# Optimization experiments

Hardware: AMD Instinct MI355X
Metric: run time of the kernel (lower is better)

## Reference

```python
import jax, jax.numpy as jnp
import numpy as np

N_ENT = 50000
N_EDGE = 600000
FEAT = 128
HID = 256
OUT = 128
TOTAL_RELS = 2 * 50 + 1  # 2*num_relations + 1
BN_EPS = 1e-5


def setup_inputs() -> dict:
    key = jax.random.key(0)
    ks = jax.random.split(key, 14)

    def xavier(k, shape):
        fan_in, fan_out = shape[0], shape[1]
        bound = float(np.sqrt(6.0 / (fan_in + fan_out)))
        return jax.random.uniform(k, shape, jnp.float32, -bound, bound)

    return {
        "edge_index": jax.random.randint(ks[0], (2, N_EDGE), 0, N_ENT, jnp.int32),
        "edge_type": jax.random.randint(ks[1], (N_EDGE,), 0, TOTAL_RELS, jnp.int32),
        "initial_features": xavier(ks[2], (N_ENT, FEAT)),
        "relation_embeddings": xavier(ks[3], (TOTAL_RELS, FEAT)),
        "W_msg": xavier(ks[4], (FEAT, HID)),
        "b_msg": jnp.zeros((HID,), jnp.float32),
        "W_self": xavier(ks[5], (FEAT, HID)),
        "W1": xavier(ks[6], (HID, HID)),
        "b1": jnp.zeros((HID,), jnp.float32),
        "gamma": jnp.ones((HID,), jnp.float32),
        "beta": jnp.zeros((HID,), jnp.float32),
        "W2": xavier(ks[7], (HID, OUT)),
        "b2": jnp.zeros((OUT,), jnp.float32),
    }


def _forward(edge_index, edge_type, initial_features, relation_embeddings,
             W_msg, b_msg, W_self, W1, b1, gamma, beta, W2, b2):
    x = initial_features                                  # [N, F]
    src, dst = edge_index[0], edge_index[1]

    # Relation-aware message: gather source feature + relation embedding per edge.
    msg = x[src] + relation_embeddings[edge_type]         # [E, F]

    # Degree-normalized scatter aggregation (mean over incoming edges).
    agg = jax.ops.segment_sum(msg, dst, num_segments=N_ENT)           # [N, F]
    deg = jax.ops.segment_sum(jnp.ones((msg.shape[0],), msg.dtype), dst,
                              num_segments=N_ENT)                     # [N]
    agg = agg / jnp.maximum(deg, 1.0)[:, None]

    # RelationGCN layer: transformed aggregate + self-loop path.
    h = agg @ W_msg + x @ W_self + b_msg                  # [N, H]

    # semantic_projector: Linear -> BatchNorm1d (batch stats) -> ReLU -> Linear.
    y = h @ W1 + b1                                       # [N, H]
    mean = jnp.mean(y, axis=0)
    var = jnp.var(y, axis=0)
    y = (y - mean) * jax.lax.rsqrt(var + BN_EPS) * gamma + beta
    y = jax.nn.relu(y)
    # Dropout omitted (deterministic reference).
    out = y @ W2 + b2                                     # [N, O]
    return out


def reference(edge_index, edge_type, initial_features, relation_embeddings,
              W_msg, b_msg, W_self, W1, b1, gamma, beta, W2, b2):
    return _forward(edge_index, edge_type, initial_features, relation_embeddings,
                    W_msg, b_msg, W_self, W1, b1, gamma, beta, W2, b2)
```

## Files before the change

kernel.cpp:

```cpp
#include <hip/hip_runtime.h>
#include <hip/hip_bf16.h>

#define N_ENT   50000
#define N_EDGE  600000
#define FEAT    128
#define HID     256
#define OUT_D   128
#define MROWS   50048
#define BN_EPS  1e-5f
#define NT32    (MROWS / 32)
#define RED_BLKS 196
#define NBUCK   196
#define EPB     4096
#define NBLK_E  147

#define OFF_SCALE   202048
#define OFF_SHIFT   203072
#define OFF_RELB    204096
#define OFF_WT1     229952
#define OFF_W1T     361024
#define OFF_W2T     492096
#define OFF_A       557632
#define OFF_Y       26182208
#define OFF_PB      52000000
#define OFF_PB2     55210000
#define OFF_ROWPTR  56000000
#define OFF_PACKED  56400064
#define OFF_EBUF    58900000
#define OFF_CHIST   61300000
#define OFF_OFFA    61420000
#define OFF_CBASE   61540000

typedef __attribute__((ext_vector_type(8))) short bf16x8;
typedef __attribute__((ext_vector_type(4))) float f32x4;

#define GLL(gp, lp) __builtin_amdgcn_global_load_lds( \
    (const __attribute__((address_space(1))) void*)(gp), \
    (__attribute__((address_space(3))) void*)(lp), 16, 0, 0)

#define MFMA(a, b, c) __builtin_amdgcn_mfma_f32_16x16x32_bf16((a), (b), (c), 0, 0, 0)

__device__ __forceinline__ ushort f2bf(float f) {
    uint u = __float_as_uint(f);
    return (ushort)((u + 0x7FFFu + ((u >> 16) & 1u)) >> 16);
}
__device__ __forceinline__ float bflo(uint u) { return __uint_as_float(u << 16); }
__device__ __forceinline__ float bfhi(uint u) { return __uint_as_float(u & 0xFFFF0000u); }

__global__ __launch_bounds__(256) void k_prep(
    const float* __restrict__ x,
    const float* __restrict__ Wm, const float* __restrict__ Wsf,
    const float* __restrict__ W1, const float* __restrict__ W2,
    const float* __restrict__ rel,
    ushort* __restrict__ A,
    ushort* __restrict__ Wt1, ushort* __restrict__ W1t,
    ushort* __restrict__ W2t, ushort* __restrict__ relb)
{
    int b = blockIdx.x;
    if (b < 3125) {
        int idx = b * 256 + threadIdx.x;
        int m = idx >> 4;
        int c = (idx & 15) * 8;
        float4 f0 = *(const float4*)(x + m * FEAT + c);
        float4 f1 = *(const float4*)(x + m * FEAT + c + 4);
        uint4 o;
        o.x = (uint)f2bf(f0.x) | ((uint)f2bf(f0.y) << 16);
        o.y = (uint)f2bf(f0.z) | ((uint)f2bf(f0.w) << 16);
        o.z = (uint)f2bf(f1.x) | ((uint)f2bf(f1.y) << 16);
        o.w = (uint)f2bf(f1.z) | ((uint)f2bf(f1.w) << 16);
        *(uint4*)(A + m * 256 + FEAT + c) = o;
    } else {
        int idx = (b - 3125) * 256 + threadIdx.x;
        if (idx < 65536) {
            int n = idx >> 8, k = idx & 255;
            float v = (k < FEAT) ? Wm[k * HID + n] : Wsf[(k - FEAT) * HID + n];
            int w = n >> 6, nb = (n >> 4) & 3, lr = n & 15;
            int kk = k >> 5, lk = (k >> 3) & 3, j = k & 7;
            int l = lk * 16 + lr;
            Wt1[(((w * 8 + kk) * 4 + nb) * 64 + l) * 8 + j] = f2bf(v);
        } else if (idx < 131072) {
            int o = idx - 65536;
            int n = o >> 8, k = o & 255;
            float v = W1[k * HID + n];
            int w = n >> 6, nb = (n >> 4) & 3, lr = n & 15;
            int kk = k >> 5, lk = (k >> 3) & 3, j = k & 7;
            int l = lk * 16 + lr;
            W1t[(((w * 8 + kk) * 4 + nb) * 64 + l) * 8 + j] = f2bf(v);
        } else if (idx < 163840) {
            int o = idx - 131072;
            int n = o >> 8, k = o & 255;
            float v = W2[k * OUT_D + n];
            int w = n >> 5, nb = (n >> 4) & 1, lr = n & 15;
            int kk = k >> 5, lk = (k >> 3) & 3, j = k & 7;
            int l = lk * 16 + lr;
            W2t[(((w * 8 + kk) * 2 + nb) * 64 + l) * 8 + j] = f2bf(v);
        } else if (idx < 163840 + 101 * 128) {
            int o = idx - 163840;
            relb[o] = f2bf(rel[o]);
        }
    }
}

__global__ __launch_bounds__(256) void k_chist(
    const int* __restrict__ ei, int* __restrict__ chist)
{
    __shared__ int h[NBUCK];
    int t = threadIdx.x;
    if (t < NBUCK) h[t] = 0;
    __syncthreads();
    #pragma unroll
    for (int r = 0; r < 16; ++r) {
        int e = (blockIdx.x * 16 + r) * 256 + t;
        if (e < N_EDGE) atomicAdd(&h[ei[N_EDGE + e] >> 8], 1);
    }
    __syncthreads();
    if (t < NBUCK) chist[blockIdx.x * NBUCK + t] = h[t];
}

__global__ __launch_bounds__(256) void k_cscan(
    const int* __restrict__ chist, int* __restrict__ offa, int* __restrict__ cbase)
{
    __shared__ int s[256];
    int k = threadIdx.x;
    int acc = 0;
    if (k < NBUCK) {
        #pragma unroll 4
        for (int b = 0; b < NBLK_E; ++b) {
            offa[b * NBUCK + k] = acc;
            acc += chist[b * NBUCK + k];
        }
    }
    s[k] = (k < NBUCK) ? acc : 0;
    int v = s[k];
    __syncthreads();
    for (int off = 1; off < 256; off <<= 1) {
        int u = (k >= off) ? s[k - off] : 0;
        __syncthreads();
        s[k] += u;
        __syncthreads();
    }
    if (k < NBUCK) cbase[k] = s[k] - v;
    if (k == NBUCK - 1) cbase[NBUCK] = s[k];
}

__global__ __launch_bounds__(256) void k_cscat(
    const int* __restrict__ ei, const int* __restrict__ et,
    const int* __restrict__ offa, const int* __restrict__ cbase,
    int* __restrict__ ebuf)
{
    __shared__ int base[NBUCK];
    int t = threadIdx.x;
    if (t < NBUCK) base[t] = offa[blockIdx.x * NBUCK + t] + cbase[t];
    __syncthreads();
    #pragma unroll
    for (int r = 0; r < 16; ++r) {
        int e = (blockIdx.x * 16 + r) * 256 + t;
        if (e < N_EDGE) {
            int dst = ei[N_EDGE + e];
            int k = dst >> 8;
            int pos = atomicAdd(&base[k], 1);
            ebuf[pos] = ei[e] | (et[e] << 16) | ((dst & 255) << 23);
        }
    }
}

__global__ __launch_bounds__(256) void k_fine(
    const int* __restrict__ ebuf, const int* __restrict__ cbase,
    int* __restrict__ rowptr, int* __restrict__ packed)
{
    __shared__ int cnt[256], sc[256];
    int t = threadIdx.x, b = blockIdx.x;
    int s0 = cbase[b], s1 = cbase[b + 1];
    cnt[t] = 0;
    __syncthreads();
    for (int e = s0 + t; e < s1; e += 256)
        atomicAdd(&cnt[(ebuf[e] >> 23) & 255], 1);
    __syncthreads();
    int v = cnt[t];
    sc[t] = v;
    __syncthreads();
    for (int off = 1; off < 256; off <<= 1) {
        int u = (t >= off) ? sc[t - off] : 0;
        __syncthreads();
        sc[t] += u;
        __syncthreads();
    }
    int ex = sc[t] - v;
    int node = b * 256 + t;
    if (node < N_ENT) rowptr[node] = s0 + ex;
    if (b == NBUCK - 1 && t == 0) rowptr[N_ENT] = s1;
    __syncthreads();
    cnt[t] = s0 + ex;
    __syncthreads();
    for (int e = s0 + t; e < s1; e += 256) {
        int v32 = ebuf[e];
        int pos = atomicAdd(&cnt[(v32 >> 23) & 255], 1);
        packed[pos] = v32 & 0x7FFFFF;
    }
}

__global__ __launch_bounds__(256) void k_agg(
    const int* __restrict__ rowptr, const int* __restrict__ packed,
    ushort* __restrict__ A, const ushort* __restrict__ relb)
{
    int node = blockIdx.x * 4 + (threadIdx.x >> 6);
    int lane = threadIdx.x & 63;
    int e0 = rowptr[node], e1 = rowptr[node + 1];
    float ax = 0.f, ay = 0.f;
    int e = e0;
    for (; e + 8 <= e1; e += 8) {
        int p0 = packed[e],     p1 = packed[e + 1], p2 = packed[e + 2], p3 = packed[e + 3];
        int p4 = packed[e + 4], p5 = packed[e + 5], p6 = packed[e + 6], p7 = packed[e + 7];
        uint xv0 = *(const uint*)(A + (p0 & 0xFFFF) * 256 + FEAT + lane * 2);
        uint rv0 = *(const uint*)(relb + (p0 >> 16) * FEAT + lane * 2);
        uint xv1 = *(const uint*)(A + (p1 & 0xFFFF) * 256 + FEAT + lane * 2);
        uint rv1 = *(const uint*)(relb + (p1 >> 16) * FEAT + lane * 2);
        uint xv2 = *(const uint*)(A + (p2 & 0xFFFF) * 256 + FEAT + lane * 2);
        uint rv2 = *(const uint*)(relb + (p2 >> 16) * FEAT + lane * 2);
        uint xv3 = *(const uint*)(A + (p3 & 0xFFFF) * 256 + FEAT + lane * 2);
        uint rv3 = *(const uint*)(relb + (p3 >> 16) * FEAT + lane * 2);
        uint xv4 = *(const uint*)(A + (p4 & 0xFFFF) * 256 + FEAT + lane * 2);
        uint rv4 = *(const uint*)(relb + (p4 >> 16) * FEAT + lane * 2);
        uint xv5 = *(const uint*)(A + (p5 & 0xFFFF) * 256 + FEAT + lane * 2);
        uint rv5 = *(const uint*)(relb + (p5 >> 16) * FEAT + lane * 2);
        uint xv6 = *(const uint*)(A + (p6 & 0xFFFF) * 256 + FEAT + lane * 2);
        uint rv6 = *(const uint*)(relb + (p6 >> 16) * FEAT + lane * 2);
        uint xv7 = *(const uint*)(A + (p7 & 0xFFFF) * 256 + FEAT + lane * 2);
        uint rv7 = *(const uint*)(relb + (p7 >> 16) * FEAT + lane * 2);
        ax += bflo(xv0) + bflo(rv0) + bflo(xv1) + bflo(rv1)
            + bflo(xv2) + bflo(rv2) + bflo(xv3) + bflo(rv3)
            + bflo(xv4) + bflo(rv4) + bflo(xv5) + bflo(rv5)
            + bflo(xv6) + bflo(rv6) + bflo(xv7) + bflo(rv7);
        ay += bfhi(xv0) + bfhi(rv0) + bfhi(xv1) + bfhi(rv1)
            + bfhi(xv2) + bfhi(rv2) + bfhi(xv3) + bfhi(rv3)
            + bfhi(xv4) + bfhi(rv4) + bfhi(xv5) + bfhi(rv5)
            + bfhi(xv6) + bfhi(rv6) + bfhi(xv7) + bfhi(rv7);
    }
    for (; e + 4 <= e1; e += 4) {
        int p0 = packed[e], p1 = packed[e + 1], p2 = packed[e + 2], p3 = packed[e + 3];
        uint xv0 = *(const uint*)(A + (p0 & 0xFFFF) * 256 + FEAT + lane * 2);
        uint rv0 = *(const uint*)(relb + (p0 >> 16) * FEAT + lane * 2);
        uint xv1 = *(const uint*)(A + (p1 & 0xFFFF) * 256 + FEAT + lane * 2);
        uint rv1 = *(const uint*)(relb + (p1 >> 16) * FEAT + lane * 2);
        uint xv2 = *(const uint*)(A + (p2 & 0xFFFF) * 256 + FEAT + lane * 2);
        uint rv2 = *(const uint*)(relb + (p2 >> 16) * FEAT + lane * 2);
        uint xv3 = *(const uint*)(A + (p3 & 0xFFFF) * 256 + FEAT + lane * 2);
        uint rv3 = *(const uint*)(relb + (p3 >> 16) * FEAT + lane * 2);
        ax += bflo(xv0) + bflo(rv0) + bflo(xv1) + bflo(rv1)
            + bflo(xv2) + bflo(rv2) + bflo(xv3) + bflo(rv3);
        ay += bfhi(xv0) + bfhi(rv0) + bfhi(xv1) + bfhi(rv1)
            + bfhi(xv2) + bfhi(rv2) + bfhi(xv3) + bfhi(rv3);
    }
    for (; e + 2 <= e1; e += 2) {
        int p0 = packed[e], p1 = packed[e + 1];
        uint xv0 = *(const uint*)(A + (p0 & 0xFFFF) * 256 + FEAT + lane * 2);
        uint rv0 = *(const uint*)(relb + (p0 >> 16) * FEAT + lane * 2);
        uint xv1 = *(const uint*)(A + (p1 & 0xFFFF) * 256 + FEAT + lane * 2);
        uint rv1 = *(const uint*)(relb + (p1 >> 16) * FEAT + lane * 2);
        ax += bflo(xv0) + bflo(rv0) + bflo(xv1) + bflo(rv1);
        ay += bfhi(xv0) + bfhi(rv0) + bfhi(xv1) + bfhi(rv1);
    }
    if (e < e1) {
        int p = packed[e];
        uint xv = *(const uint*)(A + (p & 0xFFFF) * 256 + FEAT + lane * 2);
        uint rv = *(const uint*)(relb + (p >> 16) * FEAT + lane * 2);
        ax += bflo(xv) + bflo(rv);
        ay += bfhi(xv) + bfhi(rv);
    }
    float invd = 1.0f / fmaxf((float)(e1 - e0), 1.0f);
    uint o = (uint)f2bf(ax * invd) | ((uint)f2bf(ay * invd) << 16);
    *(uint*)(A + node * 256 + lane * 2) = o;
}

__global__ __launch_bounds__(256) void k_hy(
    const ushort* __restrict__ A, const ushort* __restrict__ Wt1,
    const ushort* __restrict__ W1t,
    const float* __restrict__ bm, const float* __restrict__ b1,
    ushort* __restrict__ y, float* __restrict__ pb)
{
    __shared__ ushort a_s[32 * 256];
    int tid = threadIdx.x;
    int w = tid >> 6, l = tid & 63;
    int lr = l & 15, lk = l >> 4;
    int m0 = blockIdx.x * 32;

    {
        const ushort* srcb = A + (size_t)m0 * 256;
        #pragma unroll
        for (int j = 0; j < 4; ++j) {
            int slot = (w * 4 + j) * 64 + l;
            int lrow = slot >> 5, lgr = slot & 31;
            GLL(srcb + lrow * 256 + ((lgr ^ (lrow & 7)) << 3), &a_s[(w * 4 + j) * 512]);
        }
    }
    __syncthreads();

    f32x4 acc[2][4] = {};
    const ushort* Bp = Wt1 + w * 16384 + l * 8;
    #pragma unroll
    for (int kk = 0; kk < 8; ++kk) {
        bf16x8 a[2], b[4];
        #pragma unroll
        for (int mb = 0; mb < 2; ++mb) {
            int row = mb * 16 + lr;
            a[mb] = *(const bf16x8*)&a_s[row * 256 + (((kk * 4 + lk) ^ (lr & 7)) << 3)];
        }
        #pragma unroll
        for (int nb = 0; nb < 4; ++nb) b[nb] = *(const bf16x8*)(Bp + kk * 2048 + nb * 512);
        #pragma unroll
        for (int mb = 0; mb < 2; ++mb)
            #pragma unroll
            for (int nb = 0; nb < 4; ++nb)
                acc[mb][nb] = MFMA(a[mb], b[nb], acc[mb][nb]);
    }
    __syncthreads();

    #pragma unroll
    for (int nb = 0; nb < 4; ++nb) {
        int col = w * 64 + nb * 16 + lr;
        float bias = bm[col];
        #pragma unroll
        for (int mb = 0; mb < 2; ++mb)
            #pragma unroll
            for (int r = 0; r < 4; ++r) {
                int row = mb * 16 + lk * 4 + r;
                a_s[row * 256 + (col ^ ((row & 7) << 3))] = f2bf(acc[mb][nb][r] + bias);
            }
    }
    __syncthreads();

    f32x4 acc2[2][4] = {};
    const ushort* B2p = W1t + w * 16384 + l * 8;
    #pragma unroll
    for (int kk = 0; kk < 8; ++kk) {
        bf16x8 a[2], b[4];
        #pragma unroll
        for (int mb = 0; mb < 2; ++mb) {
            int row = mb * 16 + lr;
            a[mb] = *(const bf16x8*)&a_s[row * 256 + ((kk * 32 + lk * 8) ^ ((row & 7) << 3))];
        }
        #pragma unroll
        for (int nb = 0; nb < 4; ++nb) b[nb] = *(const bf16x8*)(B2p + kk * 2048 + nb * 512);
        #pragma unroll
        for (int mb = 0; mb < 2; ++mb)
            #pragma unroll
            for (int nb = 0; nb < 4; ++nb)
                acc2[mb][nb] = MFMA(a[mb], b[nb], acc2[mb][nb]);
    }
    __syncthreads();

    #pragma unroll
    for (int nb = 0; nb < 4; ++nb) {
        int col = w * 64 + nb * 16 + lr;
        float b1v = b1[col];
        float cs = 0.f, cq = 0.f;
        #pragma unroll
        for (int mb = 0; mb < 2; ++mb)
            #pragma unroll
            for (int r = 0; r < 4; ++r) {
                int row = mb * 16 + lk * 4 + r;
                float v = acc2[mb][nb][r] + b1v;
                if (m0 + row < N_ENT) { cs += v; cq += v * v; }
                a_s[row * 256 + (col ^ ((row & 7) << 3))] = f2bf(v);
            }
        cs += __shfl_xor(cs, 16); cs += __shfl_xor(cs, 32);
        cq += __shfl_xor(cq, 16); cq += __shfl_xor(cq, 32);
        if (lk == 0) {
            *(float2*)(pb + (size_t)blockIdx.x * 512 + col * 2) = make_float2(cs, cq);
        }
    }
    __syncthreads();
    ushort* yp = y + (size_t)m0 * 256;
    #pragma unroll
    for (int i = 0; i < 4; ++i) {
        int off = i * 2048 + tid * 8;
        *(uint4*)(yp + off) = *(const uint4*)&a_s[off];
    }
}

__global__ __launch_bounds__(256) void k_red1(
    const float* __restrict__ pb, float* __restrict__ pb2)
{
    int b = blockIdx.x, tid = threadIdx.x;
    int t0 = b * 8;
    float sx = 0.f, sy = 0.f;
    #pragma unroll
    for (int i = 0; i < 8; ++i) {
        int t = t0 + i;
        if (t < NT32) {
            float2 v = *(const float2*)(pb + (size_t)t * 512 + tid * 2);
            sx += v.x; sy += v.y;
        }
    }
    *(float2*)(pb2 + (size_t)b * 512 + tid * 2) = make_float2(sx, sy);
}

__global__ __launch_bounds__(256) void k_red2(
    const float* __restrict__ pb2,
    const float* __restrict__ gamma, const float* __restrict__ beta,
    float* __restrict__ scale, float* __restrict__ shift)
{
    int c = threadIdx.x;
    float s = 0.f, q = 0.f;
    int b = 0;
    #pragma unroll
    for (; b + 8 <= RED_BLKS; b += 8) {
        float2 v0 = *(const float2*)(pb2 + (size_t)(b + 0) * 512 + c * 2);
        float2 v1 = *(const float2*)(pb2 + (size_t)(b + 1) * 512 + c * 2);
        float2 v2 = *(const float2*)(pb2 + (size_t)(b + 2) * 512 + c * 2);
        float2 v3 = *(const float2*)(pb2 + (size_t)(b + 3) * 512 + c * 2);
        float2 v4 = *(const float2*)(pb2 + (size_t)(b + 4) * 512 + c * 2);
        float2 v5 = *(const float2*)(pb2 + (size_t)(b + 5) * 512 + c * 2);
        float2 v6 = *(const float2*)(pb2 + (size_t)(b + 6) * 512 + c * 2);
        float2 v7 = *(const float2*)(pb2 + (size_t)(b + 7) * 512 + c * 2);
        s += v0.x + v1.x + v2.x + v3.x + v4.x + v5.x + v6.x + v7.x;
        q += v0.y + v1.y + v2.y + v3.y + v4.y + v5.y + v6.y + v7.y;
    }
    for (; b < RED_BLKS; ++b) {
        float2 v = *(const float2*)(pb2 + (size_t)b * 512 + c * 2);
        s += v.x; q += v.y;
    }
    const float invn = 1.0f / (float)N_ENT;
    float mean = s * invn;
    float var  = q * invn - mean * mean;
    float rstd = rsqrtf(var + BN_EPS);
    float sc   = gamma[c] * rstd;
    scale[c] = sc;
    shift[c] = beta[c] - mean * sc;
}

__global__ __launch_bounds__(256) void k_zout(
    const ushort* __restrict__ y, const float* __restrict__ scale,
    const float* __restrict__ shift, const ushort* __restrict__ W2t,
    const float* __restrict__ b2, float* __restrict__ out)
{
    __shared__ ushort z_s[32 * 256];
    int tid = threadIdx.x;
    int w = tid >> 6, l = tid & 63;
    int lr = l & 15, lk = l >> 4;
    int m0 = blockIdx.x * 32;

    {
        const ushort* srcb = y + (size_t)m0 * 256;
        #pragma unroll
        for (int j = 0; j < 4; ++j)
            GLL(srcb + ((w * 4 + j) * 64 + l) * 8, &z_s[(w * 4 + j) * 512]);
    }
    __syncthreads();

    f32x4 acc[2][2] = {};
    const ushort* Bp = W2t + w * 8192 + l * 8;
    #pragma unroll
    for (int kk = 0; kk < 8; ++kk) {
        int kb = kk * 32 + lk * 8;
        float scv[8], shv[8];
        *(float4*)&scv[0] = *(const float4*)(scale + kb);
        *(float4*)&scv[4] = *(const float4*)(scale + kb + 4);
        *(float4*)&shv[0] = *(const float4*)(shift + kb);
        *(float4*)&shv[4] = *(const float4*)(shift + kb + 4);
        bf16x8 b[2];
        #pragma unroll
        for (int nb = 0; nb < 2; ++nb) b[nb] = *(const bf16x8*)(Bp + kk * 1024 + nb * 512);
        bf16x8 a[2];
        #pragma unroll
        for (int mb = 0; mb < 2; ++mb) {
            int row = mb * 16 + lr;
            uint4 uv = *(const uint4*)&z_s[row * 256 + (kb ^ ((row & 7) << 3))];
            uint wd[4] = {uv.x, uv.y, uv.z, uv.w};
            #pragma unroll
            for (int j = 0; j < 8; ++j) {
                uint bits = (j & 1) ? (wd[j >> 1] & 0xFFFF0000u) : (wd[j >> 1] << 16);
                float f = __uint_as_float(bits);
                float z = fmaxf(f * scv[j] + shv[j], 0.f);
                a[mb][j] = (short)f2bf(z);
            }
        }
        #pragma unroll
        for (int mb = 0; mb < 2; ++mb)
            #pragma unroll
            for (int nb = 0; nb < 2; ++nb)
                acc[mb][nb] = MFMA(a[mb], b[nb], acc[mb][nb]);
    }
    #pragma unroll
    for (int nb = 0; nb < 2; ++nb) {
        int col = w * 32 + nb * 16 + lr;
        float b2v = b2[col];
        #pragma unroll
        for (int mb = 0; mb < 2; ++mb)
            #pragma unroll
            for (int r = 0; r < 4; ++r) {
                int row = m0 + mb * 16 + lk * 4 + r;
                if (row < N_ENT) out[row * OUT_D + col] = acc[mb][nb][r] + b2v;
            }
    }
}

extern "C" void kernel_launch(void* const* d_in, const int* in_sizes, int n_in,
                              void* d_out, int out_size, void* d_ws, size_t ws_size,
                              hipStream_t stream)
{
    const int*   ei    = (const int*)d_in[0];
    const int*   et    = (const int*)d_in[1];
    const float* x     = (const float*)d_in[2];
    const float* rel   = (const float*)d_in[3];
    const float* Wm    = (const float*)d_in[4];
    const float* bm    = (const float*)d_in[5];
    const float* Wsf   = (const float*)d_in[6];
    const float* W1    = (const float*)d_in[7];
    const float* b1    = (const float*)d_in[8];
    const float* gamma = (const float*)d_in[9];
    const float* beta  = (const float*)d_in[10];
    const float* W2    = (const float*)d_in[11];
    const float* b2    = (const float*)d_in[12];
    float* out = (float*)d_out;

    char* ws = (char*)d_ws;
    float*  scale  = (float*)(ws + OFF_SCALE);
    float*  shift  = (float*)(ws + OFF_SHIFT);
    ushort* relb   = (ushort*)(ws + OFF_RELB);
    ushort* Wt1    = (ushort*)(ws + OFF_WT1);
    ushort* W1t    = (ushort*)(ws + OFF_W1T);
    ushort* W2t    = (ushort*)(ws + OFF_W2T);
    ushort* A      = (ushort*)(ws + OFF_A);
    ushort* y      = (ushort*)(ws + OFF_Y);
    float*  pb     = (float*)(ws + OFF_PB);
    float*  pb2    = (float*)(ws + OFF_PB2);
    int*    rowptr = (int*)(ws + OFF_ROWPTR);
    int*    packed = (int*)(ws + OFF_PACKED);
    int*    ebuf   = (int*)(ws + OFF_EBUF);
    int*    chist  = (int*)(ws + OFF_CHIST);
    int*    offa   = (int*)(ws + OFF_OFFA);
    int*    cbase  = (int*)(ws + OFF_CBASE);

    k_prep <<<3816, 256, 0, stream>>>(x, Wm, Wsf, W1, W2, rel, A, Wt1, W1t, W2t, relb);
    k_chist<<<NBLK_E, 256, 0, stream>>>(ei, chist);
    k_cscan<<<1, 256, 0, stream>>>(chist, offa, cbase);
    k_cscat<<<NBLK_E, 256, 0, stream>>>(ei, et, offa, cbase, ebuf);
    k_fine <<<NBUCK, 256, 0, stream>>>(ebuf, cbase, rowptr, packed);
    k_agg  <<<N_ENT / 4, 256, 0, stream>>>(rowptr, packed, A, relb);
    k_hy   <<<NT32, 256, 0, stream>>>(A, Wt1, W1t, bm, b1, y, pb);
    k_red1 <<<RED_BLKS, 256, 0, stream>>>(pb, pb2);
    k_red2 <<<1, 256, 0, stream>>>(pb2, gamma, beta, scale, shift);
    k_zout <<<NT32, 256, 0, stream>>>(y, scale, shift, W2t, b2, out);
}
```

Baseline: 151.0 us.

## Fuse histogram into prep kernel and fold bucket scan into scatter

The per-block destination histogram moves into the prep kernel as extra blocks, so it runs alongside the feature and weight conversion. The single-block scan kernel is removed. Each scatter block now re-reads the whole histogram, computes its own per-bucket offset and the global bucket bases, and block 0 writes cbase. This cuts two kernel launches and a serial single-block pass, at the cost of every scatter block redundantly reading all 147x196 histogram entries.

```diff
diff --git a/kernel.cpp b/kernel.cpp
--- a/kernel.cpp
+++ b/kernel.cpp
@@ -11,7 +11,6 @@
 #define NT32    (MROWS / 32)
 #define RED_BLKS 196
 #define NBUCK   196
-#define EPB     4096
 #define NBLK_E  147
 
 #define OFF_SCALE   202048
@@ -28,7 +27,6 @@
 #define OFF_PACKED  56400064
 #define OFF_EBUF    58900000
 #define OFF_CHIST   61300000
-#define OFF_OFFA    61420000
 #define OFF_CBASE   61540000
 
 typedef __attribute__((ext_vector_type(8))) short bf16x8;
@@ -48,17 +46,29 @@
 __device__ __forceinline__ float bfhi(uint u) { return __uint_as_float(u & 0xFFFF0000u); }
 
 __global__ __launch_bounds__(256) void k_prep(
-    const float* __restrict__ x,
+    const float* __restrict__ x, const int* __restrict__ ei,
     const float* __restrict__ Wm, const float* __restrict__ Wsf,
     const float* __restrict__ W1, const float* __restrict__ W2,
     const float* __restrict__ rel,
-    ushort* __restrict__ A,
+    ushort* __restrict__ A, int* __restrict__ chist,
     ushort* __restrict__ Wt1, ushort* __restrict__ W1t,
     ushort* __restrict__ W2t, ushort* __restrict__ relb)
 {
     int b = blockIdx.x;
-    if (b < 3125) {
-        int idx = b * 256 + threadIdx.x;
+    int t = threadIdx.x;
+    if (b < NBLK_E) {
+        __shared__ int h[NBUCK];
+        if (t < NBUCK) h[t] = 0;
+        __syncthreads();
+        #pragma unroll
+        for (int r = 0; r < 16; ++r) {
+            int e = (b * 16 + r) * 256 + t;
+            if (e < N_EDGE) atomicAdd(&h[ei[N_EDGE + e] >> 8], 1);
+        }
+        __syncthreads();
+        if (t < NBUCK) chist[b * NBUCK + t] = h[t];
+    } else if (b < NBLK_E + 3125) {
+        int idx = (b - NBLK_E) * 256 + t;
         int m = idx >> 4;
         int c = (idx & 15) * 8;
         float4 f0 = *(const float4*)(x + m * FEAT + c);
@@ -70,7 +80,7 @@
         o.w = (uint)f2bf(f1.z) | ((uint)f2bf(f1.w) << 16);
         *(uint4*)(A + m * 256 + FEAT + c) = o;
     } else {
-        int idx = (b - 3125) * 256 + threadIdx.x;
+        int idx = (b - NBLK_E - 3125) * 256 + t;
         if (idx < 65536) {
             int n = idx >> 8, k = idx & 255;
             float v = (k < FEAT) ? Wm[k * HID + n] : Wsf[(k - FEAT) * HID + n];
@@ -101,56 +111,37 @@
     }
 }
 
-__global__ __launch_bounds__(256) void k_chist(
-    const int* __restrict__ ei, int* __restrict__ chist)
-{
-    __shared__ int h[NBUCK];
+__global__ __launch_bounds__(256) void k_cscat(
+    const int* __restrict__ ei, const int* __restrict__ et,
+    const int* __restrict__ chist,
+    int* __restrict__ cbase, int* __restrict__ ebuf)
+{
+    __shared__ int base[NBUCK];
+    __shared__ int sc[256];
     int t = threadIdx.x;
-    if (t < NBUCK) h[t] = 0;
-    __syncthreads();
-    #pragma unroll
-    for (int r = 0; r < 16; ++r) {
-        int e = (blockIdx.x * 16 + r) * 256 + t;
-        if (e < N_EDGE) atomicAdd(&h[ei[N_EDGE + e] >> 8], 1);
-    }
-    __syncthreads();
-    if (t < NBUCK) chist[blockIdx.x * NBUCK + t] = h[t];
-}
-
-__global__ __launch_bounds__(256) void k_cscan(
-    const int* __restrict__ chist, int* __restrict__ offa, int* __restrict__ cbase)
-{
-    __shared__ int s[256];
-    int k = threadIdx.x;
-    int acc = 0;
-    if (k < NBUCK) {
+    int myoff = 0, total = 0;
+    if (t < NBUCK) {
         #pragma unroll 4
         for (int b = 0; b < NBLK_E; ++b) {
-            offa[b * NBUCK + k] = acc;
-            acc += chist[b * NBUCK + k];
-        }
-    }
-    s[k] = (k < NBUCK) ? acc : 0;
-    int v = s[k];
+            int c = chist[b * NBUCK + t];
+            if (b < blockIdx.x) myoff += c;
+            total += c;
+        }
+    }
+    sc[t] = (t < NBUCK) ? total : 0;
     __syncthreads();
     for (int off = 1; off < 256; off <<= 1) {
-        int u = (k >= off) ? s[k - off] : 0;
+        int u = (t >= off) ? sc[t - off] : 0;
         __syncthreads();
-        s[k] += u;
+        sc[t] += u;
         __syncthreads();
     }
-    if (k < NBUCK) cbase[k] = s[k] - v;
-    if (k == NBUCK - 1) cbase[NBUCK] = s[k];
-}
-
-__global__ __launch_bounds__(256) void k_cscat(
-    const int* __restrict__ ei, const int* __restrict__ et,
-    const int* __restrict__ offa, const int* __restrict__ cbase,
-    int* __restrict__ ebuf)
-{
-    __shared__ int base[NBUCK];
-    int t = threadIdx.x;
-    if (t < NBUCK) base[t] = offa[blockIdx.x * NBUCK + t] + cbase[t];
+    int cb_ex = sc[t] - total;
+    if (t < NBUCK) base[t] = cb_ex + myoff;
+    if (blockIdx.x == 0 && t < NBUCK) {
+        cbase[t] = cb_ex;
+        if (t == NBUCK - 1) cbase[NBUCK] = sc[t];
+    }
     __syncthreads();
     #pragma unroll
     for (int r = 0; r < 16; ++r) {
@@ -529,13 +520,11 @@
     int*    packed = (int*)(ws + OFF_PACKED);
     int*    ebuf   = (int*)(ws + OFF_EBUF);
     int*    chist  = (int*)(ws + OFF_CHIST);
-    int*    offa   = (int*)(ws + OFF_OFFA);
     int*    cbase  = (int*)(ws + OFF_CBASE);
 
-    k_prep <<<3816, 256, 0, stream>>>(x, Wm, Wsf, W1, W2, rel, A, Wt1, W1t, W2t, relb);
-    k_chist<<<NBLK_E, 256, 0, stream>>>(ei, chist);
-    k_cscan<<<1, 256, 0, stream>>>(chist, offa, cbase);
-    k_cscat<<<NBLK_E, 256, 0, stream>>>(ei, et, offa, cbase, ebuf);
+    k_prep <<<NBLK_E + 3125 + 691, 256, 0, stream>>>(x, ei, Wm, Wsf, W1, W2, rel,
+                                                     A, chist, Wt1, W1t, W2t, relb);
+    k_cscat<<<NBLK_E, 256, 0, stream>>>(ei, et, chist, cbase, ebuf);
     k_fine <<<NBUCK, 256, 0, stream>>>(ebuf, cbase, rowptr, packed);
     k_agg  <<<N_ENT / 4, 256, 0, stream>>>(rowptr, packed, A, relb);
     k_hy   <<<NT32, 256, 0, stream>>>(A, Wt1, W1t, bm, b1, y, pb);
```

Result: faster. 141.2 us (median of 2 runs) (-6.5%).
